# Optimization experiments

Hardware: AMD Instinct MI355X
Metric: run time of the kernel (lower is better)

The kernel has to match this reference:

```python
import jax, jax.numpy as jnp
import numpy as np

H = 4  # fixed number of heads in the layer


def setup_inputs() -> dict:
    key = jax.random.key(0)
    ks = jax.random.split(key, 6)
    B, S, D = 4, 2048, 512
    U = 2 * D  # per-head projection width (units = d_model * 2)
    x = jax.random.normal(ks[0], (B, S, D), dtype=jnp.float32)
    gamma = jnp.ones((D,), dtype=jnp.float32)
    beta = jnp.zeros((D,), dtype=jnp.float32)
    s = 0.02
    Wq = jax.random.normal(ks[1], (H, D, U), dtype=jnp.float32) * s
    Wk = jax.random.normal(ks[2], (H, D, U), dtype=jnp.float32) * s
    Wv = jax.random.normal(ks[3], (H, D, U), dtype=jnp.float32) * s
    Wout = jax.random.normal(ks[4], (H * U, D), dtype=jnp.float32) * s
    return {"x": x, "gamma": gamma, "beta": beta, "Wq": Wq, "Wk": Wk, "Wv": Wv, "Wout": Wout}


def _forward(x, gamma, beta, Wq, Wk, Wv, Wout):
    B, S, D = x.shape
    eps = 1e-6
    # LayerNormalization over last axis (Keras default, eps=1e-6)
    mu = jnp.mean(x, axis=-1, keepdims=True)
    var = jnp.mean(jnp.square(x - mu), axis=-1, keepdims=True)
    xn = (x - mu) * jax.lax.rsqrt(var + eps) * gamma + beta
    # Per-head Q/K/V projections, batched over head axis. Dropout is identity at inference.
    q = jnp.einsum('bsd,hdu->bhsu', xn, Wq)
    k = jnp.einsum('bsd,hdu->bhsu', xn, Wk)
    v = jnp.einsum('bsd,hdu->bhsu', xn, Wv)
    # Keras Attention(use_scale=False, causal=True): unscaled dot-product scores
    scores = jnp.einsum('bhsu,bhtu->bhst', q, k)  # [B,H,S,S]
    causal = jnp.tril(jnp.ones((S, S), dtype=bool))
    scores = jnp.where(causal, scores, jnp.finfo(scores.dtype).min)
    probs = jax.nn.softmax(scores, axis=-1)
    head = jnp.einsum('bhst,bhtu->bhsu', probs, v)  # [B,H,S,U]
    # concat heads in head order -> [B,S,H*U], then output Dense back to D
    HU = head.shape[1] * head.shape[3]
    cat = head.transpose(0, 2, 1, 3).reshape(B, S, HU)
    return cat @ Wout


def reference(x, gamma, beta, Wq, Wk, Wv, Wout):
    return _forward(x, gamma, beta, Wq, Wk, Wv, Wout)
```

## Files before the change

### kernel.cpp

```cpp
#include <hip/hip_runtime.h>

typedef _Float16 half8 __attribute__((ext_vector_type(8)));
typedef float floatx4 __attribute__((ext_vector_type(4)));

__device__ __forceinline__ void gl16(const _Float16* g, _Float16* l) {
    __builtin_amdgcn_global_load_lds((const __attribute__((address_space(1))) void*)g,
                                     (__attribute__((address_space(3))) void*)l, 16, 0, 0);
}

#define Scst 2048
#define Dcst 512
#define Ucst 1024
#define Hcst 4
#define SDo 1048576LL
#define UDo 524288LL
#define SUo 2097152LL
#define SSo 4194304LL
#define USo 2097152LL
#define SHUo 8388608LL

__global__ __launch_bounds__(64) void ln_k(const float* __restrict__ x,
                                           const float* __restrict__ gamma,
                                           const float* __restrict__ beta,
                                           _Float16* __restrict__ xn) {
    const int D = 512;
    long long base = (long long)blockIdx.x * D;
    int lane = threadIdx.x;
    floatx4 x0 = *(const floatx4*)(x + base + lane * 8);
    floatx4 x1 = *(const floatx4*)(x + base + lane * 8 + 4);
    float f[8];
#pragma unroll
    for (int i = 0; i < 4; i++) { f[i] = x0[i]; f[4 + i] = x1[i]; }
    float s = 0.f, ss = 0.f;
#pragma unroll
    for (int i = 0; i < 8; i++) { s += f[i]; ss += f[i] * f[i]; }
#pragma unroll
    for (int off = 32; off; off >>= 1) { s += __shfl_xor(s, off); ss += __shfl_xor(ss, off); }
    float mean = s * (1.f / 512.f);
    float var = ss * (1.f / 512.f) - mean * mean;
    float rstd = rsqrtf(var + 1e-6f);
    floatx4 g0 = *(const floatx4*)(gamma + lane * 8);
    floatx4 g1 = *(const floatx4*)(gamma + lane * 8 + 4);
    floatx4 b0 = *(const floatx4*)(beta + lane * 8);
    floatx4 b1 = *(const floatx4*)(beta + lane * 8 + 4);
    half8 o;
#pragma unroll
    for (int i = 0; i < 4; i++) {
        o[i]     = (_Float16)((f[i]     - mean) * rstd * g0[i] + b0[i]);
        o[4 + i] = (_Float16)((f[4 + i] - mean) * rstd * g1[i] + b1[i]);
    }
    *(half8*)(xn + base + lane * 8) = o;
}

__global__ __launch_bounds__(256) void tr_k(const float* __restrict__ in,
                                            _Float16* __restrict__ out, int R, int C) {
    __shared__ _Float16 tile[32][33];
    int tx = threadIdx.x, ty = threadIdx.y;
    long long zo = (long long)blockIdx.z * R * C;
    int r0 = blockIdx.y * 32, c0 = blockIdx.x * 32;
    for (int yy = ty; yy < 32; yy += 8)
        tile[yy][tx] = (_Float16)in[zo + (long long)(r0 + yy) * C + c0 + tx];
    __syncthreads();
    for (int yy = ty; yy < 32; yy += 8)
        out[zo + (long long)(c0 + yy) * R + r0 + tx] = tile[tx][yy];
}

#define BM 128
#define BN 128
#define BK 32
__global__ __launch_bounds__(256) void gemm_bt(
    const _Float16* __restrict__ A, const _Float16* __restrict__ Bt, void* __restrict__ Cv,
    int K, int ldc, int cflags, int mode) {
    int z = blockIdx.z;
    long long offA = 0, offB = 0, offC = 0;
    switch (mode) {
        case 1:
            offA = (long long)((z >> 2) & 1) * SDo;
            offB = (long long)(((z >> 3) * 4) + (z & 3)) * UDo;
            offC = (long long)(((z >> 3) * 8) + ((z & 3) * 2) + ((z >> 2) & 1)) * SUo;
            break;
        case 2:
            offA = (long long)z * SUo; offB = (long long)z * SUo; offC = (long long)z * SSo;
            break;
        case 3:
            offA = (long long)(z >> 1) * UDo; offB = (long long)(z & 1) * SDo;
            offC = (long long)z * USo;
            break;
        case 4:
            offA = (long long)z * SSo; offB = (long long)z * USo;
            offC = (long long)(z & 1) * SHUo + (long long)(z >> 1) * Ucst;
            break;
        case 6:
            offB = (long long)(z & 7) * UDo; offC = (long long)z * SUo;
            break;
        case 7:
            offA = (long long)(z & 3) * UDo; offC = (long long)z * USo;
            break;
        default: break;
    }
    const _Float16* Ab = A + offA;
    const _Float16* Bb = Bt + offB;

    int gx = gridDim.x, gy = gridDim.y;
    int nb = gx * gy;
    int lin = blockIdx.y * gx + blockIdx.x;
    int mIdx, nIdx;
    if (((nb & 7) == 0) && ((gx & 3) == 0)) {
        int chunk = nb >> 3;
        int vid = (lin >> 3) + chunk * (lin & 7);
        int panelH = gy * 4;
        int panel = vid / panelH;
        int rem = vid - panel * panelH;
        mIdx = rem >> 2;
        nIdx = (panel << 2) + (rem & 3);
    } else { mIdx = blockIdx.y; nIdx = blockIdx.x; }
    int m0 = mIdx * BM, n0 = nIdx * BN;

    if ((cflags & 4) && n0 > m0 + (BM - 1)) return;
    int kend = (cflags & 8) ? min(K, m0 + BM) : K;

    __shared__ _Float16 As[2][BM * BK];
    __shared__ _Float16 Bs[2][BN * BK];

    int t = threadIdx.x;
    int srow = t >> 2;
    int scol = (t & 3) * 8;
    int lane = t & 63, w = t >> 6;
    int wm = (w >> 1) * 64, wn = (w & 1) * 64;
    int lm = lane & 15, lk = (lane >> 4) * 8;

    floatx4 acc[4][4];
#pragma unroll
    for (int i = 0; i < 4; i++)
#pragma unroll
        for (int j = 0; j < 4; j++) acc[i][j] = floatx4{0.f, 0.f, 0.f, 0.f};

    const _Float16* ga0 = Ab + (long long)(m0 + srow) * K + scol;
    const _Float16* ga1 = Ab + (long long)(m0 + 64 + srow) * K + scol;
    const _Float16* gb0 = Bb + (long long)(n0 + srow) * K + scol;
    const _Float16* gb1 = Bb + (long long)(n0 + 64 + srow) * K + scol;

    int nIter = kend / BK;
    gl16(ga0, &As[0][t * 8]);
    gl16(ga1, &As[0][2048 + t * 8]);
    gl16(gb0, &Bs[0][t * 8]);
    gl16(gb1, &Bs[0][2048 + t * 8]);

    for (int it = 0; it < nIter; it++) {
        __syncthreads();
        int cur = it & 1;
        half8 af[4], bfr[4];
#pragma unroll
        for (int i = 0; i < 4; i++) af[i] = *(const half8*)&As[cur][(wm + i * 16 + lm) * BK + lk];
#pragma unroll
        for (int j = 0; j < 4; j++) bfr[j] = *(const half8*)&Bs[cur][(wn + j * 16 + lm) * BK + lk];
        if (it + 1 < nIter) {
            int nk = (it + 1) * BK;
            int nxt = cur ^ 1;
            gl16(ga0 + nk, &As[nxt][t * 8]);
            gl16(ga1 + nk, &As[nxt][2048 + t * 8]);
            gl16(gb0 + nk, &Bs[nxt][t * 8]);
            gl16(gb1 + nk, &Bs[nxt][2048 + t * 8]);
        }
#pragma unroll
        for (int i = 0; i < 4; i++)
#pragma unroll
            for (int j = 0; j < 4; j++)
                acc[i][j] = __builtin_amdgcn_mfma_f32_16x16x32_f16(af[i], bfr[j], acc[i][j], 0, 0, 0);
    }

    int cr = (lane >> 4) * 4;
    int cc = lm;
    bool outf32 = (cflags & 1) != 0;
#pragma unroll
    for (int i = 0; i < 4; i++) {
#pragma unroll
        for (int j = 0; j < 4; j++) {
            int rr = m0 + wm + i * 16 + cr;
            int nn = n0 + wn + j * 16 + cc;
#pragma unroll
            for (int r2 = 0; r2 < 4; r2++) {
                long long idx = (long long)(rr + r2) * ldc + nn + offC;
                float val = acc[i][j][r2];
                if (outf32) ((float*)Cv)[idx] = val;
                else ((_Float16*)Cv)[idx] = (_Float16)val;
            }
        }
    }
}

__global__ __launch_bounds__(256) void softmax_h(_Float16* __restrict__ sc, int S) {
    int wid = threadIdx.x >> 6, lane = threadIdx.x & 63;
    int idx = blockIdx.x * 4 + wid;
    int r = idx & (S - 1);
    _Float16* srow = sc + (long long)idx * S;
    int nc = r >> 9;
    float v[32];
    float mx = -3.0e38f;
    for (int c = 0; c <= nc; c++) {
        half8 hv = *(half8*)(srow + lane * 8 + c * 512);
#pragma unroll
        for (int i = 0; i < 8; i++) {
            int n = lane * 8 + c * 512 + i;
            float s = (n <= r) ? (float)hv[i] : -3.0e38f;
            v[c * 8 + i] = s; mx = fmaxf(mx, s);
        }
    }
#pragma unroll
    for (int off = 32; off; off >>= 1) mx = fmaxf(mx, __shfl_xor(mx, off));
    float sum = 0.f;
    for (int c = 0; c <= nc; c++)
#pragma unroll
        for (int i = 0; i < 8; i++) {
            int n = lane * 8 + c * 512 + i;
            float e = (n <= r) ? __expf(v[c * 8 + i] - mx) : 0.f;
            v[c * 8 + i] = e; sum += e;
        }
#pragma unroll
    for (int off = 32; off; off >>= 1) sum += __shfl_xor(sum, off);
    float inv = 1.f / sum;
    for (int c = 0; c <= nc; c++) {
        half8 o;
#pragma unroll
        for (int i = 0; i < 8; i++) o[i] = (_Float16)(v[c * 8 + i] * inv);
        *(half8*)(srow + lane * 8 + c * 512) = o;
    }
}

extern "C" void kernel_launch(void* const* d_in, const int* in_sizes, int n_in,
                              void* d_out, int out_size, void* d_ws, size_t ws_size,
                              hipStream_t stream) {
    const int B = 4, S = 2048, D = 512, H = 4, U = 1024;
    const float* x     = (const float*)d_in[0];
    const float* gamma = (const float*)d_in[1];
    const float* beta  = (const float*)d_in[2];
    const float* Wq    = (const float*)d_in[3];
    const float* Wk    = (const float*)d_in[4];
    const float* Wv    = (const float*)d_in[5];
    const float* Wout  = (const float*)d_in[6];
    float* out = (float*)d_out;

    char* ws = (char*)d_ws;
    const size_t MiB = 1ull << 20;
    const long long SD = SDo, UD = UDo, SU = SUo, US = USo;

    _Float16* xn  = (_Float16*)(ws + 0);
    _Float16* WqT = (_Float16*)(ws + 8  * MiB);
    _Float16* WkT = (_Float16*)(ws + 12 * MiB);
    _Float16* WvT = (_Float16*)(ws + 16 * MiB);
    _Float16* WoT = (_Float16*)(ws + 20 * MiB);

    tr_k<<<dim3(U / 32, D / 32, H), dim3(32, 8), 0, stream>>>(Wq, WqT, D, U);
    tr_k<<<dim3(U / 32, D / 32, H), dim3(32, 8), 0, stream>>>(Wk, WkT, D, U);
    tr_k<<<dim3(U / 32, D / 32, H), dim3(32, 8), 0, stream>>>(Wv, WvT, D, U);
    tr_k<<<dim3(D / 32, (H * U) / 32, 1), dim3(32, 8), 0, stream>>>(Wout, WoT, H * U, D);
    ln_k<<<B * S, 64, 0, stream>>>(x, gamma, beta, xn);

    if (ws_size >= 168 * MiB) {
        _Float16* qk  = (_Float16*)(ws + 24 * MiB);
        _Float16* kk  = qk + 8 * SU;
        _Float16* sc  = (_Float16*)(ws + 88 * MiB);
        _Float16* vt  = qk;
        _Float16* cat = kk;

        for (int p = 0; p < 2; p++) {
            const _Float16* xnp = xn + (long long)p * 2 * SD;
            float* outp = out + (long long)p * 2 * SD;
            gemm_bt<<<dim3(U / 128, S / 128, 16), 256, 0, stream>>>(xnp, WqT, qk, D, U, 0, 1);
            gemm_bt<<<dim3(S / 128, S / 128, 8), 256, 0, stream>>>(qk, kk, sc, U, S, 4, 2);
            softmax_h<<<8 * S / 4, 256, 0, stream>>>(sc, S);
            gemm_bt<<<dim3(S / 128, U / 128, 8), 256, 0, stream>>>(WvT, xnp, vt, D, S, 0, 3);
            gemm_bt<<<dim3(U / 128, S / 128, 8), 256, 0, stream>>>(sc, vt, cat, S, H * U, 8, 4);
            gemm_bt<<<dim3(D / 128, 2 * S / 128, 1), 256, 0, stream>>>(cat, WoT, outp,
                H * U, D, 1, 0);
        }
    } else {
        _Float16* qb   = (_Float16*)(ws + 24 * MiB);
        _Float16* vTb  = (_Float16*)(ws + 56 * MiB);
        _Float16* catb = (_Float16*)(ws + 72 * MiB);
        _Float16* sc   = (_Float16*)(ws + 88 * MiB);

        for (int b = 0; b < B; b++) {
            const _Float16* xnb = xn + (long long)b * SD;
            gemm_bt<<<dim3(U / 128, S / 128, 2 * H), 256, 0, stream>>>(xnb, WqT, qb, D, U, 0, 6);
            gemm_bt<<<dim3(S / 128, U / 128, H), 256, 0, stream>>>(WvT, xnb, vTb, D, S, 0, 7);
            for (int h = 0; h < H; h++) {
                gemm_bt<<<dim3(S / 128, S / 128, 1), 256, 0, stream>>>(qb + (long long)h * SU,
                    qb + (long long)(H + h) * SU, sc, U, S, 4, 0);
                softmax_h<<<S / 4, 256, 0, stream>>>(sc, S);
                gemm_bt<<<dim3(U / 128, S / 128, 1), 256, 0, stream>>>(sc,
                    vTb + (long long)h * US, (void*)(catb + (long long)h * U), S, H * U, 8, 0);
            }
            gemm_bt<<<dim3(D / 128, S / 128, 1), 256, 0, stream>>>(catb, WoT,
                (void*)(out + (long long)b * SD), H * U, D, 1, 0);
        }
    }
}
```

Baseline: 742.6 us.

## Replace 4-wave GEMM with single-wave 64x64 tile kernel using waitcnt pipelining

Replaces the 256-thread 128x128 GEMM with a 64-thread single-wavefront kernel that computes a 64x64 tile. The kernel keeps two LDS buffers filled by direct global-to-LDS loads and orders them with explicit s_waitcnt instead of __syncthreads. This removes block barriers and yields four times as many blocks for better occupancy and load balance on the causal tiles. In exchange, each block reuses less data per tile, so global and L2 traffic per FLOP roughly doubles, and correctness depends on the hand-coded waitcnt encodings.

```diff
diff --git a/kernel.cpp b/kernel.cpp
--- a/kernel.cpp
+++ b/kernel.cpp
@@ -8,10 +8,7 @@
                                      (__attribute__((address_space(3))) void*)l, 16, 0, 0);
 }
 
-#define Scst 2048
-#define Dcst 512
 #define Ucst 1024
-#define Hcst 4
 #define SDo 1048576LL
 #define UDo 524288LL
 #define SUo 2097152LL
@@ -65,10 +62,19 @@
         out[zo + (long long)(c0 + yy) * R + r0 + tx] = tile[tx][yy];
 }
 
-#define BM 128
-#define BN 128
-#define BK 32
-__global__ __launch_bounds__(256) void gemm_bt(
+__device__ __forceinline__ void stage8(const _Float16* a, const _Float16* b,
+                                       _Float16* Ad, _Float16* Bd, int t, long long rs16) {
+    gl16(a,            Ad + t * 8);
+    gl16(a + rs16,     Ad + 512 + t * 8);
+    gl16(a + 2 * rs16, Ad + 1024 + t * 8);
+    gl16(a + 3 * rs16, Ad + 1536 + t * 8);
+    gl16(b,            Bd + t * 8);
+    gl16(b + rs16,     Bd + 512 + t * 8);
+    gl16(b + 2 * rs16, Bd + 1024 + t * 8);
+    gl16(b + 3 * rs16, Bd + 1536 + t * 8);
+}
+
+__global__ __launch_bounds__(64) void gemm_w(
     const _Float16* __restrict__ A, const _Float16* __restrict__ Bt, void* __restrict__ Cv,
     int K, int ldc, int cflags, int mode) {
     int z = blockIdx.z;
@@ -114,20 +120,21 @@
         mIdx = rem >> 2;
         nIdx = (panel << 2) + (rem & 3);
     } else { mIdx = blockIdx.y; nIdx = blockIdx.x; }
-    int m0 = mIdx * BM, n0 = nIdx * BN;
-
-    if ((cflags & 4) && n0 > m0 + (BM - 1)) return;
-    int kend = (cflags & 8) ? min(K, m0 + BM) : K;
-
-    __shared__ _Float16 As[2][BM * BK];
-    __shared__ _Float16 Bs[2][BN * BK];
+    int m0 = mIdx * 64, n0 = nIdx * 64;
+
+    if ((cflags & 4) && n0 > m0 + 63) return;
+    int kend = (cflags & 8) ? min(K, m0 + 64) : K;
+
+    __shared__ _Float16 As0[2048];
+    __shared__ _Float16 As1[2048];
+    __shared__ _Float16 Bs0[2048];
+    __shared__ _Float16 Bs1[2048];
 
     int t = threadIdx.x;
-    int srow = t >> 2;
-    int scol = (t & 3) * 8;
-    int lane = t & 63, w = t >> 6;
-    int wm = (w >> 1) * 64, wn = (w & 1) * 64;
-    int lm = lane & 15, lk = (lane >> 4) * 8;
+    int lm = t & 15, lk = (t >> 4) * 8;
+    long long rs16 = 16LL * K;
+    const _Float16* gA = Ab + (long long)(m0 + (t >> 2)) * K + (t & 3) * 8;
+    const _Float16* gB = Bb + (long long)(n0 + (t >> 2)) * K + (t & 3) * 8;
 
     floatx4 acc[4][4];
 #pragma unroll
@@ -135,49 +142,51 @@
 #pragma unroll
         for (int j = 0; j < 4; j++) acc[i][j] = floatx4{0.f, 0.f, 0.f, 0.f};
 
-    const _Float16* ga0 = Ab + (long long)(m0 + srow) * K + scol;
-    const _Float16* ga1 = Ab + (long long)(m0 + 64 + srow) * K + scol;
-    const _Float16* gb0 = Bb + (long long)(n0 + srow) * K + scol;
-    const _Float16* gb1 = Bb + (long long)(n0 + 64 + srow) * K + scol;
-
-    int nIter = kend / BK;
-    gl16(ga0, &As[0][t * 8]);
-    gl16(ga1, &As[0][2048 + t * 8]);
-    gl16(gb0, &Bs[0][t * 8]);
-    gl16(gb1, &Bs[0][2048 + t * 8]);
-
-    for (int it = 0; it < nIter; it++) {
-        __syncthreads();
-        int cur = it & 1;
-        half8 af[4], bfr[4];
-#pragma unroll
-        for (int i = 0; i < 4; i++) af[i] = *(const half8*)&As[cur][(wm + i * 16 + lm) * BK + lk];
-#pragma unroll
-        for (int j = 0; j < 4; j++) bfr[j] = *(const half8*)&Bs[cur][(wn + j * 16 + lm) * BK + lk];
-        if (it + 1 < nIter) {
-            int nk = (it + 1) * BK;
-            int nxt = cur ^ 1;
-            gl16(ga0 + nk, &As[nxt][t * 8]);
-            gl16(ga1 + nk, &As[nxt][2048 + t * 8]);
-            gl16(gb0 + nk, &Bs[nxt][t * 8]);
-            gl16(gb1 + nk, &Bs[nxt][2048 + t * 8]);
-        }
+    int nIter = kend / 32;
+    stage8(gA, gB, As0, Bs0, t, rs16);
+    stage8(gA + 32, gB + 32, As1, Bs1, t, rs16);
+
+    for (int it = 0; it < nIter; it += 2) {
+        __builtin_amdgcn_s_waitcnt(0x0F78);
+        half8 a0[4], b0[4];
+#pragma unroll
+        for (int i = 0; i < 4; i++) a0[i] = *(const half8*)&As0[(i * 16 + lm) * 32 + lk];
+#pragma unroll
+        for (int j = 0; j < 4; j++) b0[j] = *(const half8*)&Bs0[(j * 16 + lm) * 32 + lk];
+        __builtin_amdgcn_s_waitcnt(0xC07F);
+        bool s2 = (it + 2) < nIter;
+        if (s2) stage8(gA + (it + 2) * 32, gB + (it + 2) * 32, As0, Bs0, t, rs16);
 #pragma unroll
         for (int i = 0; i < 4; i++)
 #pragma unroll
             for (int j = 0; j < 4; j++)
-                acc[i][j] = __builtin_amdgcn_mfma_f32_16x16x32_f16(af[i], bfr[j], acc[i][j], 0, 0, 0);
-    }
-
-    int cr = (lane >> 4) * 4;
+                acc[i][j] = __builtin_amdgcn_mfma_f32_16x16x32_f16(a0[i], b0[j], acc[i][j], 0, 0, 0);
+        if (s2) __builtin_amdgcn_s_waitcnt(0x0F78);
+        else    __builtin_amdgcn_s_waitcnt(0x0F70);
+        half8 a1[4], b1[4];
+#pragma unroll
+        for (int i = 0; i < 4; i++) a1[i] = *(const half8*)&As1[(i * 16 + lm) * 32 + lk];
+#pragma unroll
+        for (int j = 0; j < 4; j++) b1[j] = *(const half8*)&Bs1[(j * 16 + lm) * 32 + lk];
+        __builtin_amdgcn_s_waitcnt(0xC07F);
+        if ((it + 3) < nIter)
+            stage8(gA + (it + 3) * 32, gB + (it + 3) * 32, As1, Bs1, t, rs16);
+#pragma unroll
+        for (int i = 0; i < 4; i++)
+#pragma unroll
+            for (int j = 0; j < 4; j++)
+                acc[i][j] = __builtin_amdgcn_mfma_f32_16x16x32_f16(a1[i], b1[j], acc[i][j], 0, 0, 0);
+    }
+
+    int cr = (t >> 4) * 4;
     int cc = lm;
     bool outf32 = (cflags & 1) != 0;
 #pragma unroll
     for (int i = 0; i < 4; i++) {
 #pragma unroll
         for (int j = 0; j < 4; j++) {
-            int rr = m0 + wm + i * 16 + cr;
-            int nn = n0 + wn + j * 16 + cc;
+            int rr = m0 + i * 16 + cr;
+            int nn = n0 + j * 16 + cc;
 #pragma unroll
             for (int r2 = 0; r2 < 4; r2++) {
                 long long idx = (long long)(rr + r2) * ldc + nn + offC;
@@ -242,7 +251,7 @@
 
     char* ws = (char*)d_ws;
     const size_t MiB = 1ull << 20;
-    const long long SD = SDo, UD = UDo, SU = SUo, US = USo;
+    const long long SD = SDo, SU = SUo, US = USo;
 
     _Float16* xn  = (_Float16*)(ws + 0);
     _Float16* WqT = (_Float16*)(ws + 8  * MiB);
@@ -266,12 +275,12 @@
         for (int p = 0; p < 2; p++) {
             const _Float16* xnp = xn + (long long)p * 2 * SD;
             float* outp = out + (long long)p * 2 * SD;
-            gemm_bt<<<dim3(U / 128, S / 128, 16), 256, 0, stream>>>(xnp, WqT, qk, D, U, 0, 1);
-            gemm_bt<<<dim3(S / 128, S / 128, 8), 256, 0, stream>>>(qk, kk, sc, U, S, 4, 2);
+            gemm_w<<<dim3(U / 64, S / 64, 16), 64, 0, stream>>>(xnp, WqT, qk, D, U, 0, 1);
+            gemm_w<<<dim3(S / 64, S / 64, 8), 64, 0, stream>>>(qk, kk, sc, U, S, 4, 2);
             softmax_h<<<8 * S / 4, 256, 0, stream>>>(sc, S);
-            gemm_bt<<<dim3(S / 128, U / 128, 8), 256, 0, stream>>>(WvT, xnp, vt, D, S, 0, 3);
-            gemm_bt<<<dim3(U / 128, S / 128, 8), 256, 0, stream>>>(sc, vt, cat, S, H * U, 8, 4);
-            gemm_bt<<<dim3(D / 128, 2 * S / 128, 1), 256, 0, stream>>>(cat, WoT, outp,
+            gemm_w<<<dim3(S / 64, U / 64, 8), 64, 0, stream>>>(WvT, xnp, vt, D, S, 0, 3);
+            gemm_w<<<dim3(U / 64, S / 64, 8), 64, 0, stream>>>(sc, vt, cat, S, H * U, 8, 4);
+            gemm_w<<<dim3(D / 64, 2 * S / 64, 1), 64, 0, stream>>>(cat, WoT, outp,
                 H * U, D, 1, 0);
         }
     } else {
@@ -282,16 +291,16 @@
 
         for (int b = 0; b < B; b++) {
             const _Float16* xnb = xn + (long long)b * SD;
-            gemm_bt<<<dim3(U / 128, S / 128, 2 * H), 256, 0, stream>>>(xnb, WqT, qb, D, U, 0, 6);
-            gemm_bt<<<dim3(S / 128, U / 128, H), 256, 0, stream>>>(WvT, xnb, vTb, D, S, 0, 7);
+            gemm_w<<<dim3(U / 64, S / 64, 2 * H), 64, 0, stream>>>(xnb, WqT, qb, D, U, 0, 6);
+            gemm_w<<<dim3(S / 64, U / 64, H), 64, 0, stream>>>(WvT, xnb, vTb, D, S, 0, 7);
             for (int h = 0; h < H; h++) {
-                gemm_bt<<<dim3(S / 128, S / 128, 1), 256, 0, stream>>>(qb + (long long)h * SU,
+                gemm_w<<<dim3(S / 64, S / 64, 1), 64, 0, stream>>>(qb + (long long)h * SU,
                     qb + (long long)(H + h) * SU, sc, U, S, 4, 0);
                 softmax_h<<<S / 4, 256, 0, stream>>>(sc, S);
-                gemm_bt<<<dim3(U / 128, S / 128, 1), 256, 0, stream>>>(sc,
+                gemm_w<<<dim3(U / 64, S / 64, 1), 64, 0, stream>>>(sc,
                     vTb + (long long)h * US, (void*)(catb + (long long)h * U), S, H * U, 8, 0);
             }
-            gemm_bt<<<dim3(D / 128, S / 128, 1), 256, 0, stream>>>(catb, WoT,
+            gemm_w<<<dim3(D / 64, S / 64, 1), 64, 0, stream>>>(catb, WoT,
                 (void*)(out + (long long)b * SD), H * U, D, 1, 0);
         }
     }
```

Measured after the change: 918.7 us. 23.7% more time.
